# Kernel tuning notes

Measured on AMD Instinct MI355X. Metric: run time of the kernel, lower is better.

The kernel has to match this reference:

```python
import jax, jax.numpy as jnp
import numpy as np

N = 50000        # nodes
E = 800000       # edges (avg degree 16)
G = 64           # graphs in batch
F_IN = 9
OUT = 10


def setup_inputs() -> dict:
    key = jax.random.key(0)
    ks = jax.random.split(key, 20)
    def w(k, fi, fo):
        return jax.random.normal(k, (fi, fo), dtype=jnp.float32) * (1.0 / np.sqrt(fi))
    inp = {
        "x": jax.random.normal(ks[0], (N, F_IN), dtype=jnp.float32),
        "edge_index": jax.random.randint(ks[1], (2, E), 0, N, dtype=jnp.int64),
        "batch": jnp.sort(jax.random.randint(ks[2], (N,), 0, G, dtype=jnp.int64)),
        # GCNConv weights (PyG: x @ W then normalized scatter-add, + bias)
        "W1": w(ks[3], F_IN, 128), "b1": jnp.zeros((128,), jnp.float32),
        "W2": w(ks[4], 128, 256),  "b2": jnp.zeros((256,), jnp.float32),
        "W3": w(ks[5], 256, 256),  "b3": jnp.zeros((256,), jnp.float32),
        "W4": w(ks[6], 256, 256),  "b4": jnp.zeros((256,), jnp.float32),
        # dense head
        "Wl2": w(ks[7], 256, 128), "bl2": jnp.zeros((128,), jnp.float32),
        "Wl3": w(ks[8], 128, 128), "bl3": jnp.zeros((128,), jnp.float32),
        "Wl":  w(ks[9], 128, OUT), "bl":  jnp.zeros((OUT,), jnp.float32),
    }
    return inp


def reference(x, edge_index, batch, W1, b1, W2, b2, W3, b3, W4, b4,
              Wl2, bl2, Wl3, bl3, Wl, bl):
    # GCNConv with self-loops and symmetric deg^{-1/2} normalization
    loops = jnp.arange(N, dtype=edge_index.dtype)
    src = jnp.concatenate([edge_index[0], loops])   # [E+N]
    dst = jnp.concatenate([edge_index[1], loops])
    deg = jax.ops.segment_sum(jnp.ones_like(src, dtype=x.dtype), dst, num_segments=N)
    dinv = jax.lax.rsqrt(deg)                        # deg >= 1 due to self-loops
    norm = (dinv[src] * dinv[dst])[:, None]          # [E+N, 1]

    def conv(h, W, b):
        msg = (h @ W)[src] * norm                    # gather + normalize
        return jax.ops.segment_sum(msg, dst, num_segments=N) + b

    h = jax.nn.relu(conv(x, W1, b1))
    h = jax.nn.relu(conv(h, W2, b2))
    h = jax.nn.relu(conv(h, W3, b3))
    h = conv(h, W4, b4)                              # no relu before pool
    g = jax.ops.segment_max(h, batch, num_segments=G)  # global_max_pool -> [G, 256]
    g = jax.nn.relu(g @ Wl2 + bl2)
    g = jax.nn.relu(g @ Wl3 + bl3)
    out = g @ Wl + bl                                # [G, OUT]
    return jnp.squeeze(out)
```

## Files before the change

### kernel.cpp

```cpp
#include <hip/hip_runtime.h>
#include <float.h>

#define NN 50000
#define NE 800000
#define NG 64
#define CAP 64
#define EPT 16

typedef __attribute__((ext_vector_type(8))) _Float16 f16x8;
typedef __attribute__((ext_vector_type(4))) float f32x4;
typedef __attribute__((ext_vector_type(4))) _Float16 half4;
typedef unsigned int u32;
typedef unsigned short u16;

__device__ __forceinline__ unsigned f2mono(float f) {
  unsigned b = __float_as_uint(f);
  return (b & 0x80000000u) ? ~b : (b | 0x80000000u);
}
__device__ __forceinline__ float mono2f(unsigned u) {
  unsigned b = (u & 0x80000000u) ? (u & 0x7fffffffu) : ~u;
  return __uint_as_float(b);
}
__device__ __forceinline__ void gl_lds16(const void* g, void* l) {
  __builtin_amdgcn_global_load_lds((const __attribute__((address_space(1))) u32*)g,
                                   (__attribute__((address_space(3))) u32*)l, 16, 0, 0);
}

__global__ __launch_bounds__(256) void k_count(const int* __restrict__ src,
                                               const int* __restrict__ dst,
                                               int* __restrict__ cnt,
                                               u16* __restrict__ col) {
  int s = blockIdx.x & 7;
  int base = (blockIdx.x >> 3) * (256 * EPT) + threadIdx.x;
#pragma unroll
  for (int r = 0; r < EPT; ++r) {
    int e = base + r * 256;
    if (e >= NE) break;
    int d = dst[e];
    if ((d & 7) != s) continue;
    if ((unsigned)d >= NN) continue;
    int sv = src[e];
    if ((unsigned)sv >= NN) continue;
    int pos = atomicAdd(&cnt[d], 1);
    if (pos < CAP) col[d * CAP + pos] = (u16)sv;
  }
}

__global__ void k_dinv(const int* __restrict__ cnt, float* __restrict__ dinv,
                       const float* __restrict__ x, float* __restrict__ xs,
                       unsigned* __restrict__ g) {
  int v = blockIdx.x * blockDim.x + threadIdx.x;
  if (v >= NN) return;
  if (v < NG * 256) g[v] = 0u;
  float d = rsqrtf((float)cnt[v] + 1.0f);
  dinv[v] = d;
#pragma unroll
  for (int i = 0; i < 9; ++i) xs[v * 9 + i] = x[v * 9 + i] * d;
}

__device__ __forceinline__ void splitw1(const float* W, _Float16* Wh, _Float16* Wl,
                                        int i, int K, int Nc) {
  int k = i / Nc, n = i - k * Nc;
  float w = W[i];
  _Float16 h = (_Float16)w;
  _Float16 l = (_Float16)(w - (float)h);
  Wh[(size_t)n * K + k] = h;
  Wl[(size_t)n * K + k] = l;
}
__global__ void k_splitw3(const float* __restrict__ W2, const float* __restrict__ W3,
                          const float* __restrict__ W4,
                          _Float16* __restrict__ W2h, _Float16* __restrict__ W2l,
                          _Float16* __restrict__ W3h, _Float16* __restrict__ W3l,
                          _Float16* __restrict__ W4h, _Float16* __restrict__ W4l) {
  int i = blockIdx.x * 256 + threadIdx.x;
  const int n2 = 128 * 256, n3 = 256 * 256;
  if (i < n2) splitw1(W2, W2h, W2l, i, 128, 256);
  else if (i < n2 + n3) splitw1(W3, W3h, W3l, i - n2, 256, 256);
  else if (i < n2 + 2 * n3) splitw1(W4, W4h, W4l, i - n2 - n3, 256, 256);
}

__global__ __launch_bounds__(256) void k_agg9(const float* __restrict__ xs,
                                              float* __restrict__ out,
                                              const int* __restrict__ cnt,
                                              const u16* __restrict__ col,
                                              const float* __restrict__ dinv) {
  int v = (blockIdx.x * 256 + threadIdx.x) >> 4;
  int l = threadIdx.x & 15;
  if (v >= NN) return;
  int c = cnt[v]; if (c > CAP) c = CAP;
  const u16* cl = col + (size_t)v * CAP;
  float acc = (l < 9) ? xs[v * 9 + l] : 0.0f;
  int j = 0;
  for (; j + 4 <= c; j += 4) {
    ushort4 u = *(const ushort4*)(cl + j);
    float a0 = (l < 9) ? xs[(int)u.x * 9 + l] : 0.f;
    float a1 = (l < 9) ? xs[(int)u.y * 9 + l] : 0.f;
    float a2 = (l < 9) ? xs[(int)u.z * 9 + l] : 0.f;
    float a3 = (l < 9) ? xs[(int)u.w * 9 + l] : 0.f;
    acc += (a0 + a1) + (a2 + a3);
  }
  for (; j < c; ++j) {
    int u = cl[j];
    if (l < 9) acc += xs[u * 9 + l];
  }
  if (l < 9) out[v * 9 + l] = acc * dinv[v];
}

__global__ __launch_bounds__(256) void k_gemm9(const float* __restrict__ in,
                                               const float* __restrict__ W,
                                               const float* __restrict__ bias,
                                               const float* __restrict__ dinv,
                                               _Float16* __restrict__ out) {
  __shared__ float sW[9 * 128];
  __shared__ float sb[128];
  int t = threadIdx.x;
  if (t < 128) sb[t] = bias[t];
  for (int i = t; i < 9 * 128; i += 256) sW[i] = W[i];
  __syncthreads();
  int r = blockIdx.x * 2 + (t >> 7);
  int c = t & 127;
  if (r >= NN) return;
  float acc = sb[c];
#pragma unroll
  for (int i = 0; i < 9; ++i) acc += in[r * 9 + i] * sW[i * 128 + c];
  out[r * 128 + c] = (_Float16)(fmaxf(acc, 0.0f) * dinv[r]);
}

__global__ __launch_bounds__(256) void k_aggs(const half4* __restrict__ h,
                                              half4* __restrict__ out,
                                              const int* __restrict__ cnt,
                                              const u16* __restrict__ col,
                                              const float* __restrict__ dinv,
                                              int rowU, int slog) {
  int bid = blockIdx.x;
  int s = bid & ((1 << slog) - 1);
  int chunk = bid >> slog;
  int g = threadIdx.x >> 4;
  int l = threadIdx.x & 15;
  int v = chunk * 16 + g;
  if (v >= NN) return;
  int so = s * 16 + l;
  int c = cnt[v]; if (c > CAP) c = CAP;
  const u16* cl = col + (size_t)v * CAP;
  half4 sv = h[(size_t)v * rowU + so];
  float ax = (float)sv.x, ay = (float)sv.y, az = (float)sv.z, aw = (float)sv.w;
  int j = 0;
  for (; j + 4 <= c; j += 4) {
    ushort4 u = *(const ushort4*)(cl + j);
    half4 t0 = h[(size_t)u.x * rowU + so];
    half4 t1 = h[(size_t)u.y * rowU + so];
    half4 t2 = h[(size_t)u.z * rowU + so];
    half4 t3 = h[(size_t)u.w * rowU + so];
    ax += ((float)t0.x + (float)t1.x) + ((float)t2.x + (float)t3.x);
    ay += ((float)t0.y + (float)t1.y) + ((float)t2.y + (float)t3.y);
    az += ((float)t0.z + (float)t1.z) + ((float)t2.z + (float)t3.z);
    aw += ((float)t0.w + (float)t1.w) + ((float)t2.w + (float)t3.w);
  }
  for (; j < c; ++j) {
    half4 tv = h[(size_t)cl[j] * rowU + so];
    ax += (float)tv.x; ay += (float)tv.y; az += (float)tv.z; aw += (float)tv.w;
  }
  float d = dinv[v];
  half4 o;
  o.x = (_Float16)(ax * d); o.y = (_Float16)(ay * d);
  o.z = (_Float16)(az * d); o.w = (_Float16)(aw * d);
  out[(size_t)v * rowU + so] = o;
}

__global__ __launch_bounds__(256) void k_mm(const _Float16* __restrict__ A,
                                            const _Float16* __restrict__ Bh,
                                            const _Float16* __restrict__ Bl,
                                            const float* __restrict__ bias,
                                            _Float16* __restrict__ C,
                                            const float* __restrict__ dinv,
                                            const int* __restrict__ batch,
                                            unsigned* __restrict__ gpool,
                                            int M, int K, int Nc, int mode) {
  __shared__ __align__(16) _Float16 Alds[128 * 64];
  __shared__ __align__(16) _Float16 Bhl[128 * 64];
  __shared__ __align__(16) _Float16 Bll[128 * 64];
  int bid = blockIdx.x;
  int rblk = (bid >> 4) * 8 + (bid & 7);
  int cblk = (bid >> 3) & 1;
  if (rblk * 128 >= M) return;
  int rowBase = rblk * 128;
  int colBase = cblk * 128;
  int t = threadIdx.x;
  int wave = t >> 6, lane = t & 63;
  int wm = wave & 1, wn = wave >> 1;
  int lm = lane & 15;
  int q  = lane >> 4;

  int srl = wave * 32 + (lane >> 3);
  int sj  = lane & 7;
  int ssw = lane >> 3;
  int gseg = sj ^ ssw;

  f32x4 acc[4][4];
#pragma unroll
  for (int i = 0; i < 4; ++i)
#pragma unroll
    for (int j = 0; j < 4; ++j) acc[i][j] = (f32x4){0.f, 0.f, 0.f, 0.f};

  int nit = K >> 6;
  for (int it = 0; it < nit; ++it) {
    __syncthreads();
#pragma unroll
    for (int c = 0; c < 4; ++c) {
      int rl = srl + c * 8;
      int ga = rowBase + rl; if (ga > M - 1) ga = M - 1;
      int gb = colBase + rl;
      unsigned off = (unsigned)it * 64 + gseg * 8;
      int ldst = (wave * 32 + c * 8) * 64 + lane * 8;
      gl_lds16(A  + (size_t)ga * K + off, Alds + ldst);
      gl_lds16(Bh + (size_t)gb * K + off, Bhl + ldst);
      gl_lds16(Bl + (size_t)gb * K + off, Bll + ldst);
    }
    __syncthreads();

#pragma unroll
    for (int s2 = 0; s2 < 2; ++s2) {
      int slotq = ((s2 << 2) | q);
      f16x8 vbh[4], vbl[4];
#pragma unroll
      for (int ni = 0; ni < 4; ++ni) {
        int rB = wn * 64 + ni * 16 + lm;
        int slot = slotq ^ (lm & 7);
        vbh[ni] = *(const f16x8*)(Bhl + rB * 64 + slot * 8);
        vbl[ni] = *(const f16x8*)(Bll + rB * 64 + slot * 8);
      }
#pragma unroll
      for (int mi = 0; mi < 4; ++mi) {
        int rA = wm * 64 + mi * 16 + lm;
        int slot = slotq ^ (lm & 7);
        f16x8 va = *(const f16x8*)(Alds + rA * 64 + slot * 8);
#pragma unroll
        for (int ni = 0; ni < 4; ++ni) {
          acc[mi][ni] = __builtin_amdgcn_mfma_f32_16x16x32_f16(va, vbh[ni], acc[mi][ni], 0, 0, 0);
          acc[mi][ni] = __builtin_amdgcn_mfma_f32_16x16x32_f16(va, vbl[ni], acc[mi][ni], 0, 0, 0);
        }
      }
    }
  }

  int rowOff = (lane >> 4) * 4;
  if (mode == 2) {
    __syncthreads();
    unsigned* ldsPool = (unsigned*)Alds;
    for (int i = t; i < 4 * 256; i += 256) ldsPool[i] = 0u;
    __syncthreads();
    int b0 = batch[rowBase];
#pragma unroll
    for (int mi = 0; mi < 4; ++mi) {
#pragma unroll
      for (int ni = 0; ni < 4; ++ni) {
        int gc = colBase + wn * 64 + ni * 16 + lm;
        float bsv = bias[gc];
#pragma unroll
        for (int r = 0; r < 4; ++r) {
          int gr = rowBase + wm * 64 + mi * 16 + rowOff + r;
          if (gr < M) {
            float v = acc[mi][ni][r] + bsv;
            int idx = batch[gr] - b0;
            if (idx < 0) idx = 0;
            if (idx > 3) idx = 3;
            atomicMax(&ldsPool[idx * 256 + gc], f2mono(v));
          }
        }
      }
    }
    __syncthreads();
#pragma unroll
    for (int s4 = 0; s4 < 4; ++s4) {
      unsigned mv = ldsPool[s4 * 256 + t];
      int gb = b0 + s4;
      if (mv && gb < NG) atomicMax(&gpool[gb * 256 + t], mv);
    }
  } else {
#pragma unroll
    for (int mi = 0; mi < 4; ++mi) {
#pragma unroll
      for (int ni = 0; ni < 4; ++ni) {
        int gc = colBase + wn * 64 + ni * 16 + lm;
        float bsv = bias[gc];
#pragma unroll
        for (int r = 0; r < 4; ++r) {
          int gr = rowBase + wm * 64 + mi * 16 + rowOff + r;
          if (gr < M) {
            float v = fmaxf(acc[mi][ni][r] + bsv, 0.0f);
            C[(size_t)gr * Nc + gc] = (_Float16)(v * dinv[gr]);
          }
        }
      }
    }
  }
}

__global__ __launch_bounds__(256) void k_head(const unsigned* __restrict__ g,
                                              const float* __restrict__ Wl2, const float* __restrict__ bl2,
                                              const float* __restrict__ Wl3, const float* __restrict__ bl3,
                                              const float* __restrict__ Wl, const float* __restrict__ bl,
                                              float* __restrict__ out) {
  __shared__ float s0[256];
  __shared__ float s1[128];
  __shared__ float s2[128];
  int b = blockIdx.x, t = threadIdx.x;
  s0[t] = mono2f(g[b * 256 + t]);
  __syncthreads();
  if (t < 128) {
    float acc = bl2[t];
    for (int k = 0; k < 256; ++k) acc += s0[k] * Wl2[k * 128 + t];
    s1[t] = fmaxf(acc, 0.0f);
  }
  __syncthreads();
  if (t < 128) {
    float acc = bl3[t];
    for (int k = 0; k < 128; ++k) acc += s1[k] * Wl3[k * 128 + t];
    s2[t] = fmaxf(acc, 0.0f);
  }
  __syncthreads();
  if (t < 10) {
    float acc = bl[t];
    for (int k = 0; k < 128; ++k) acc += s2[k] * Wl[k * 10 + t];
    out[b * 10 + t] = acc;
  }
}

extern "C" void kernel_launch(void* const* d_in, const int* in_sizes, int n_in,
                              void* d_out, int out_size, void* d_ws, size_t ws_size,
                              hipStream_t stream) {
  const float* x   = (const float*)d_in[0];
  const int* eidx  = (const int*)d_in[1];
  const int* batch = (const int*)d_in[2];
  const float* W1 = (const float*)d_in[3];   const float* b1 = (const float*)d_in[4];
  const float* W2 = (const float*)d_in[5];   const float* b2 = (const float*)d_in[6];
  const float* W3 = (const float*)d_in[7];   const float* b3 = (const float*)d_in[8];
  const float* W4 = (const float*)d_in[9];   const float* b4 = (const float*)d_in[10];
  const float* Wl2 = (const float*)d_in[11]; const float* bl2 = (const float*)d_in[12];
  const float* Wl3 = (const float*)d_in[13]; const float* bl3 = (const float*)d_in[14];
  const float* Wl  = (const float*)d_in[15]; const float* bl  = (const float*)d_in[16];
  float* out = (float*)d_out;

  _Float16* bufA = (_Float16*)d_ws;
  _Float16* bufB = bufA + (size_t)NN * 256;
  int* cnt  = (int*)(bufB + (size_t)NN * 256);
  float* dinv = (float*)(cnt + NN);
  u16* col  = (u16*)(dinv + NN);
  unsigned* g = (unsigned*)(col + (size_t)NN * CAP);
  _Float16* W2h = (_Float16*)(g + NG * 256);
  _Float16* W2l = W2h + 256 * 128;
  _Float16* W3h = W2l + 256 * 128;
  _Float16* W3l = W3h + 256 * 256;
  _Float16* W4h = W3l + 256 * 256;
  _Float16* W4l = W4h + 256 * 256;
  float* xs = (float*)bufA;
  float* agg9out = (float*)bufB;

  const int* src = eidx;
  const int* dst = eidx + NE;

  hipMemsetAsync(cnt, 0, NN * sizeof(int), stream);

  const int cntGrid = 8 * ((NE + 256 * EPT - 1) / (256 * EPT));
  k_count<<<cntGrid, 256, 0, stream>>>(src, dst, cnt, col);
  k_dinv<<<(NN + 255) / 256, 256, 0, stream>>>(cnt, dinv, x, xs, g);

  k_splitw3<<<(128 * 256 + 2 * 256 * 256 + 255) / 256, 256, 0, stream>>>(
      W2, W3, W4, W2h, W2l, W3h, W3l, W4h, W4l);

  k_agg9<<<(NN + 15) / 16, 256, 0, stream>>>(xs, agg9out, cnt, col, dinv);
  k_gemm9<<<NN / 2, 256, 0, stream>>>(agg9out, W1, b1, dinv, bufA);

  const int nchunk = (NN + 15) / 16;
  const int mmGrid = 784;

  k_aggs<<<nchunk * 2, 256, 0, stream>>>((const half4*)bufA, (half4*)bufB, cnt, col, dinv, 32, 1);
  k_mm<<<mmGrid, 256, 0, stream>>>(bufB, W2h, W2l, b2, bufA, dinv, batch, g, NN, 128, 256, 1);

  k_aggs<<<nchunk * 4, 256, 0, stream>>>((const half4*)bufA, (half4*)bufB, cnt, col, dinv, 64, 2);
  k_mm<<<mmGrid, 256, 0, stream>>>(bufB, W3h, W3l, b3, bufA, dinv, batch, g, NN, 256, 256, 1);

  k_aggs<<<nchunk * 4, 256, 0, stream>>>((const half4*)bufA, (half4*)bufB, cnt, col, dinv, 64, 2);
  k_mm<<<mmGrid, 256, 0, stream>>>(bufB, W4h, W4l, b4, bufA, dinv, batch, g, NN, 256, 256, 2);

  k_head<<<NG, 256, 0, stream>>>(g, Wl2, bl2, Wl3, bl3, Wl, bl, out);
}
```

Baseline: 425.4 us.

## Fuse neighbor aggregation into GEMM kernel with full-width 256-column tiles

Replaces the separate gather-aggregate kernel and MFMA GEMM kernel with a single fused kernel. Each 512-thread block aggregates neighbor features for its 128 rows directly into LDS for each K-slice, then multiplies against all 256 output columns, streaming the hi and lo weight halves through one shared buffer. This removes the intermediate aggregated-feature round trip to global memory and cuts kernel launches. The trade-off is that gathers now sit in the GEMM critical path with little latency hiding, and the grid shrinks to about 391 blocks.

```diff
diff --git a/kernel.cpp b/kernel.cpp
--- a/kernel.cpp
+++ b/kernel.cpp
@@ -126,75 +126,32 @@
   out[r * 128 + c] = (_Float16)(fmaxf(acc, 0.0f) * dinv[r]);
 }
 
-__global__ __launch_bounds__(256) void k_aggs(const half4* __restrict__ h,
-                                              half4* __restrict__ out,
-                                              const int* __restrict__ cnt,
-                                              const u16* __restrict__ col,
-                                              const float* __restrict__ dinv,
-                                              int rowU, int slog) {
-  int bid = blockIdx.x;
-  int s = bid & ((1 << slog) - 1);
-  int chunk = bid >> slog;
-  int g = threadIdx.x >> 4;
-  int l = threadIdx.x & 15;
-  int v = chunk * 16 + g;
-  if (v >= NN) return;
-  int so = s * 16 + l;
-  int c = cnt[v]; if (c > CAP) c = CAP;
-  const u16* cl = col + (size_t)v * CAP;
-  half4 sv = h[(size_t)v * rowU + so];
-  float ax = (float)sv.x, ay = (float)sv.y, az = (float)sv.z, aw = (float)sv.w;
-  int j = 0;
-  for (; j + 4 <= c; j += 4) {
-    ushort4 u = *(const ushort4*)(cl + j);
-    half4 t0 = h[(size_t)u.x * rowU + so];
-    half4 t1 = h[(size_t)u.y * rowU + so];
-    half4 t2 = h[(size_t)u.z * rowU + so];
-    half4 t3 = h[(size_t)u.w * rowU + so];
-    ax += ((float)t0.x + (float)t1.x) + ((float)t2.x + (float)t3.x);
-    ay += ((float)t0.y + (float)t1.y) + ((float)t2.y + (float)t3.y);
-    az += ((float)t0.z + (float)t1.z) + ((float)t2.z + (float)t3.z);
-    aw += ((float)t0.w + (float)t1.w) + ((float)t2.w + (float)t3.w);
-  }
-  for (; j < c; ++j) {
-    half4 tv = h[(size_t)cl[j] * rowU + so];
-    ax += (float)tv.x; ay += (float)tv.y; az += (float)tv.z; aw += (float)tv.w;
-  }
-  float d = dinv[v];
-  half4 o;
-  o.x = (_Float16)(ax * d); o.y = (_Float16)(ay * d);
-  o.z = (_Float16)(az * d); o.w = (_Float16)(aw * d);
-  out[(size_t)v * rowU + so] = o;
-}
-
-__global__ __launch_bounds__(256) void k_mm(const _Float16* __restrict__ A,
-                                            const _Float16* __restrict__ Bh,
-                                            const _Float16* __restrict__ Bl,
-                                            const float* __restrict__ bias,
-                                            _Float16* __restrict__ C,
-                                            const float* __restrict__ dinv,
-                                            const int* __restrict__ batch,
-                                            unsigned* __restrict__ gpool,
-                                            int M, int K, int Nc, int mode) {
+__global__ __launch_bounds__(512, 4) void k_aggmm(
+    const _Float16* __restrict__ h,
+    const _Float16* __restrict__ Bh,
+    const _Float16* __restrict__ Bl,
+    const float* __restrict__ bias,
+    _Float16* __restrict__ C,
+    const float* __restrict__ dinv,
+    const int* __restrict__ cnt,
+    const u16* __restrict__ col,
+    const int* __restrict__ batch,
+    unsigned* __restrict__ gpool,
+    int K, int mode) {
   __shared__ __align__(16) _Float16 Alds[128 * 64];
-  __shared__ __align__(16) _Float16 Bhl[128 * 64];
-  __shared__ __align__(16) _Float16 Bll[128 * 64];
-  int bid = blockIdx.x;
-  int rblk = (bid >> 4) * 8 + (bid & 7);
-  int cblk = (bid >> 3) & 1;
-  if (rblk * 128 >= M) return;
-  int rowBase = rblk * 128;
-  int colBase = cblk * 128;
+  __shared__ __align__(16) _Float16 Bst[256 * 64];
+  int rowBase = blockIdx.x * 128;
   int t = threadIdx.x;
   int wave = t >> 6, lane = t & 63;
   int wm = wave & 1, wn = wave >> 1;
-  int lm = lane & 15;
-  int q  = lane >> 4;
-
-  int srl = wave * 32 + (lane >> 3);
+  int lm = lane & 15, q = lane >> 4;
+  int ssw = lane >> 3;
   int sj  = lane & 7;
-  int ssw = lane >> 3;
   int gseg = sj ^ ssw;
+  int grp = t >> 4;
+  int gl  = t & 15;
+  int rowU4 = K >> 2;
+  const half4* h4 = (const half4*)h;
 
   f32x4 acc[4][4];
 #pragma unroll
@@ -207,59 +164,101 @@
     __syncthreads();
 #pragma unroll
     for (int c = 0; c < 4; ++c) {
-      int rl = srl + c * 8;
-      int ga = rowBase + rl; if (ga > M - 1) ga = M - 1;
-      int gb = colBase + rl;
-      unsigned off = (unsigned)it * 64 + gseg * 8;
-      int ldst = (wave * 32 + c * 8) * 64 + lane * 8;
-      gl_lds16(A  + (size_t)ga * K + off, Alds + ldst);
-      gl_lds16(Bh + (size_t)gb * K + off, Bhl + ldst);
-      gl_lds16(Bl + (size_t)gb * K + off, Bll + ldst);
-    }
-    __syncthreads();
-
+      int rb = wave * 32 + c * 8;
+      gl_lds16(Bh + (size_t)(rb + ssw) * K + it * 64 + gseg * 8,
+               Bst + rb * 64 + lane * 8);
+    }
+    int kb4 = it * 16;
+#pragma unroll
+    for (int ri = 0; ri < 4; ++ri) {
+      int rr = grp + ri * 32;
+      int v = rowBase + rr; if (v > NN - 1) v = NN - 1;
+      int c = cnt[v]; if (c > CAP) c = CAP;
+      const u16* cl = col + (size_t)v * CAP;
+      size_t hoff = kb4 + gl;
+      half4 sv = h4[(size_t)v * rowU4 + hoff];
+      float ax = (float)sv.x, ay = (float)sv.y, az = (float)sv.z, aw = (float)sv.w;
+      for (int j = 0; j < c; j += 4) {
+        ushort4 u = *(const ushort4*)(cl + j);
+        int i0 = (j + 0 < c) ? (int)u.x : v;
+        int i1 = (j + 1 < c) ? (int)u.y : v;
+        int i2 = (j + 2 < c) ? (int)u.z : v;
+        int i3 = (j + 3 < c) ? (int)u.w : v;
+        half4 t0 = h4[(size_t)i0 * rowU4 + hoff];
+        half4 t1 = h4[(size_t)i1 * rowU4 + hoff];
+        half4 t2 = h4[(size_t)i2 * rowU4 + hoff];
+        half4 t3 = h4[(size_t)i3 * rowU4 + hoff];
+        if (j + 0 < c) { ax += (float)t0.x; ay += (float)t0.y; az += (float)t0.z; aw += (float)t0.w; }
+        if (j + 1 < c) { ax += (float)t1.x; ay += (float)t1.y; az += (float)t1.z; aw += (float)t1.w; }
+        if (j + 2 < c) { ax += (float)t2.x; ay += (float)t2.y; az += (float)t2.z; aw += (float)t2.w; }
+        if (j + 3 < c) { ax += (float)t3.x; ay += (float)t3.y; az += (float)t3.z; aw += (float)t3.w; }
+      }
+      float d = dinv[v];
+      half4 o;
+      o.x = (_Float16)(ax * d); o.y = (_Float16)(ay * d);
+      o.z = (_Float16)(az * d); o.w = (_Float16)(aw * d);
+      ((half4*)Alds)[rr * 16 + (((gl >> 1) ^ (rr & 7)) << 1) + (gl & 1)] = o;
+    }
+    __syncthreads();
 #pragma unroll
     for (int s2 = 0; s2 < 2; ++s2) {
-      int slotq = ((s2 << 2) | q);
-      f16x8 vbh[4], vbl[4];
+      int slotq = (s2 << 2) | q;
+      int slot = slotq ^ (lm & 7);
+      f16x8 va[4];
+#pragma unroll
+      for (int mi = 0; mi < 4; ++mi)
+        va[mi] = *(const f16x8*)(Alds + (wm * 64 + mi * 16 + lm) * 64 + slot * 8);
 #pragma unroll
       for (int ni = 0; ni < 4; ++ni) {
-        int rB = wn * 64 + ni * 16 + lm;
-        int slot = slotq ^ (lm & 7);
-        vbh[ni] = *(const f16x8*)(Bhl + rB * 64 + slot * 8);
-        vbl[ni] = *(const f16x8*)(Bll + rB * 64 + slot * 8);
-      }
-#pragma unroll
-      for (int mi = 0; mi < 4; ++mi) {
-        int rA = wm * 64 + mi * 16 + lm;
-        int slot = slotq ^ (lm & 7);
-        f16x8 va = *(const f16x8*)(Alds + rA * 64 + slot * 8);
-#pragma unroll
-        for (int ni = 0; ni < 4; ++ni) {
-          acc[mi][ni] = __builtin_amdgcn_mfma_f32_16x16x32_f16(va, vbh[ni], acc[mi][ni], 0, 0, 0);
-          acc[mi][ni] = __builtin_amdgcn_mfma_f32_16x16x32_f16(va, vbl[ni], acc[mi][ni], 0, 0, 0);
-        }
-      }
-    }
-  }
-
-  int rowOff = (lane >> 4) * 4;
+        f16x8 vb = *(const f16x8*)(Bst + (wn * 64 + ni * 16 + lm) * 64 + slot * 8);
+#pragma unroll
+        for (int mi = 0; mi < 4; ++mi)
+          acc[mi][ni] = __builtin_amdgcn_mfma_f32_16x16x32_f16(va[mi], vb, acc[mi][ni], 0, 0, 0);
+      }
+    }
+    __syncthreads();
+#pragma unroll
+    for (int c = 0; c < 4; ++c) {
+      int rb = wave * 32 + c * 8;
+      gl_lds16(Bl + (size_t)(rb + ssw) * K + it * 64 + gseg * 8,
+               Bst + rb * 64 + lane * 8);
+    }
+    __syncthreads();
+#pragma unroll
+    for (int s2 = 0; s2 < 2; ++s2) {
+      int slotq = (s2 << 2) | q;
+      int slot = slotq ^ (lm & 7);
+      f16x8 va[4];
+#pragma unroll
+      for (int mi = 0; mi < 4; ++mi)
+        va[mi] = *(const f16x8*)(Alds + (wm * 64 + mi * 16 + lm) * 64 + slot * 8);
+#pragma unroll
+      for (int ni = 0; ni < 4; ++ni) {
+        f16x8 vb = *(const f16x8*)(Bst + (wn * 64 + ni * 16 + lm) * 64 + slot * 8);
+#pragma unroll
+        for (int mi = 0; mi < 4; ++mi)
+          acc[mi][ni] = __builtin_amdgcn_mfma_f32_16x16x32_f16(va[mi], vb, acc[mi][ni], 0, 0, 0);
+      }
+    }
+  }
+
+  int rowOff = q * 4;
   if (mode == 2) {
     __syncthreads();
     unsigned* ldsPool = (unsigned*)Alds;
-    for (int i = t; i < 4 * 256; i += 256) ldsPool[i] = 0u;
+    for (int i = t; i < 4 * 256; i += 512) ldsPool[i] = 0u;
     __syncthreads();
     int b0 = batch[rowBase];
 #pragma unroll
     for (int mi = 0; mi < 4; ++mi) {
 #pragma unroll
       for (int ni = 0; ni < 4; ++ni) {
-        int gc = colBase + wn * 64 + ni * 16 + lm;
+        int gc = wn * 64 + ni * 16 + lm;
         float bsv = bias[gc];
 #pragma unroll
         for (int r = 0; r < 4; ++r) {
           int gr = rowBase + wm * 64 + mi * 16 + rowOff + r;
-          if (gr < M) {
+          if (gr < NN) {
             float v = acc[mi][ni][r] + bsv;
             int idx = batch[gr] - b0;
             if (idx < 0) idx = 0;
@@ -270,25 +269,25 @@
       }
     }
     __syncthreads();
-#pragma unroll
-    for (int s4 = 0; s4 < 4; ++s4) {
-      unsigned mv = ldsPool[s4 * 256 + t];
+    int tc = t & 255, th = t >> 8;
+    for (int s4 = th; s4 < 4; s4 += 2) {
+      unsigned mv = ldsPool[s4 * 256 + tc];
       int gb = b0 + s4;
-      if (mv && gb < NG) atomicMax(&gpool[gb * 256 + t], mv);
+      if (mv && gb < NG) atomicMax(&gpool[gb * 256 + tc], mv);
     }
   } else {
 #pragma unroll
     for (int mi = 0; mi < 4; ++mi) {
 #pragma unroll
       for (int ni = 0; ni < 4; ++ni) {
-        int gc = colBase + wn * 64 + ni * 16 + lm;
+        int gc = wn * 64 + ni * 16 + lm;
         float bsv = bias[gc];
 #pragma unroll
         for (int r = 0; r < 4; ++r) {
           int gr = rowBase + wm * 64 + mi * 16 + rowOff + r;
-          if (gr < M) {
+          if (gr < NN) {
             float v = fmaxf(acc[mi][ni][r] + bsv, 0.0f);
-            C[(size_t)gr * Nc + gc] = (_Float16)(v * dinv[gr]);
+            C[(size_t)gr * 256 + gc] = (_Float16)(v * dinv[gr]);
           }
         }
       }
@@ -371,17 +370,11 @@
   k_agg9<<<(NN + 15) / 16, 256, 0, stream>>>(xs, agg9out, cnt, col, dinv);
   k_gemm9<<<NN / 2, 256, 0, stream>>>(agg9out, W1, b1, dinv, bufA);
 
-  const int nchunk = (NN + 15) / 16;
-  const int mmGrid = 784;
-
-  k_aggs<<<nchunk * 2, 256, 0, stream>>>((const half4*)bufA, (half4*)bufB, cnt, col, dinv, 32, 1);
-  k_mm<<<mmGrid, 256, 0, stream>>>(bufB, W2h, W2l, b2, bufA, dinv, batch, g, NN, 128, 256, 1);
-
-  k_aggs<<<nchunk * 4, 256, 0, stream>>>((const half4*)bufA, (half4*)bufB, cnt, col, dinv, 64, 2);
-  k_mm<<<mmGrid, 256, 0, stream>>>(bufB, W3h, W3l, b3, bufA, dinv, batch, g, NN, 256, 256, 1);
-
-  k_aggs<<<nchunk * 4, 256, 0, stream>>>((const half4*)bufA, (half4*)bufB, cnt, col, dinv, 64, 2);
-  k_mm<<<mmGrid, 256, 0, stream>>>(bufB, W4h, W4l, b4, bufA, dinv, batch, g, NN, 256, 256, 2);
+  const int fGrid = (NN + 127) / 128;
+
+  k_aggmm<<<fGrid, 512, 0, stream>>>(bufA, W2h, W2l, b2, bufB, dinv, cnt, col, batch, g, 128, 1);
+  k_aggmm<<<fGrid, 512, 0, stream>>>(bufB, W3h, W3l, b3, bufA, dinv, cnt, col, batch, g, 256, 1);
+  k_aggmm<<<fGrid, 512, 0, stream>>>(bufA, W4h, W4l, b4, bufB, dinv, cnt, col, batch, g, 256, 2);
 
   k_head<<<NG, 256, 0, stream>>>(g, Wl2, bl2, Wl3, bl3, Wl, bl, out);
 }
```

After: 690.2 us. 1.62x slower.
